# Kernel optimization log

Measured on AMD Instinct MI355X. Metric: run time of the kernel, lower is better.

Reference implementation:

```python
import jax, jax.numpy as jnp
import numpy as np

E_DIM = 64
N_EMBED = 8192

def setup_inputs() -> dict:
    key = jax.random.key(0)
    k1, k2 = jax.random.split(key)
    x = jax.random.normal(k1, (16, E_DIM, 32, 32), dtype=jnp.float32)   # [B, e_dim, H, W]
    embed = jax.random.normal(k2, (E_DIM, N_EMBED), dtype=jnp.float32)  # codebook [e_dim, n_embed]
    return {"x": x, "embed": embed}

def reference(x, embed):
    e_dim, n_embed = embed.shape
    # NCHW -> NHWC
    xp = jnp.transpose(x, (0, 2, 3, 1))              # [B, H, W, e_dim]
    flat = xp.reshape(-1, e_dim)                     # [N, e_dim]
    # squared-distance expansion: ||f||^2 - 2 f.E + ||e||^2  -> [N, n_embed]
    distance = (jnp.sum(flat * flat, axis=1, keepdims=True)
                - 2.0 * flat @ embed
                + jnp.sum(embed * embed, axis=0, keepdims=True))
    embed_idx = jnp.argmax(-distance, axis=1)        # [N] nearest code ids
    embed_idx = embed_idx.reshape(xp.shape[:-1])     # [B, H, W]
    # gather codes: embedding table is embed.T -> [n_embed, e_dim]
    quantize = jnp.take(embed.T, embed_idx, axis=0)  # [B, H, W, e_dim]
    return quantize
```

## Files before the change

### kernel.cpp

```cpp
#include <hip/hip_runtime.h>


typedef __attribute__((ext_vector_type(8))) __bf16 bf16x8;
typedef __attribute__((ext_vector_type(4))) float f32x4;
typedef unsigned int u32;
typedef unsigned long long u64;

union frag_cast { f32x4 f; bf16x8 b; };
__device__ __forceinline__ bf16x8 as_bf16x8(f32x4 v) { frag_cast u; u.f = v; return u.b; }

#define N_ROWS  16384
#define E_DIM   64
#define N_EMBED 8192
#define NCHUNK  16
#define COLS_PER_BLOCK (N_EMBED / NCHUNK)
#define N_ST (COLS_PER_BLOCK / 64)
#define ROWS_PER_BLOCK 512
#define N_ROWBLK (N_ROWS / ROWS_PER_BLOCK)
#define NT 8
#define MARGIN_THR 2e-3f

#define WS_AH   0u
#define WS_AL   (2u << 20)
#define WS_B    (4u << 20)
#define WS_ET   (6u << 20)
#define WS_BIAS (8u << 20)
#define WS_CNT  (WS_BIAS + (32u << 10))
#define WS_PB1  (WS_CNT + (4u << 10))
#define WS_PI1  (WS_PB1 + (1u << 20))
#define WS_PB2  (WS_PI1 + (1u << 20))
#define WS_FLAG (WS_PB2 + (1u << 20))
#define WS_FKEY (WS_FLAG + (64u << 10))
#define WS_DONE (WS_FKEY + (128u << 10))

__device__ __forceinline__ u32 f32_key(float s) {
    u32 u = __float_as_uint(s);
    return (u & 0x80000000u) ? ~u : (u | 0x80000000u);
}

__device__ __forceinline__ void async16(const void* g, void* l) {
    __builtin_amdgcn_global_load_lds(
        (const __attribute__((address_space(1))) void*)g,
        (__attribute__((address_space(3))) void*)l, 16, 0, 0);
}

__global__ __launch_bounds__(256) void prep(
        const float* __restrict__ x, const float* __restrict__ embed, char* ws) {
    __shared__ float tile[64][65];
    __bf16* Ah = (__bf16*)(ws + WS_AH);
    __bf16* Al = (__bf16*)(ws + WS_AL);
    float*  eT = (float*)(ws + WS_ET);
    float*  bias = (float*)(ws + WS_BIAS);
    const int t = threadIdx.x;
    const int blk = blockIdx.x;

    if (blk < 256) {
        const int b = blk >> 4, p0 = (blk & 15) * 64;
        {
            const int c = t >> 2, seg = (t & 3) * 16;
            const float* src = x + b * 65536 + c * 1024 + p0 + seg;
#pragma unroll
            for (int i = 0; i < 16; ++i) tile[c][seg + i] = src[i];
        }
        __syncthreads();
        const int p = t >> 2, cq = (t & 3) * 16;
        const long row = b * 1024 + p0 + p;
        bf16x8 vh0, vh1, vl0, vl1;
#pragma unroll
        for (int i = 0; i < 16; ++i) {
            float f = tile[cq + i][p];
            __bf16 h = (__bf16)f;
            __bf16 l = (__bf16)(f - (float)h);
            if (i < 8) { vh0[i] = h; vl0[i] = l; }
            else       { vh1[i - 8] = h; vl1[i - 8] = l; }
        }
        *(bf16x8*)(Ah + row * 64 + cq) = vh0;
        *(bf16x8*)(Ah + row * 64 + cq + 8) = vh1;
        *(bf16x8*)(Al + row * 64 + cq) = vl0;
        *(bf16x8*)(Al + row * 64 + cq + 8) = vl1;
    } else {
        if (blk == 256 && t == 0) *(int*)(ws + WS_CNT) = 0;
        const int g = blk - 256;
        const int jbase = g * 64;
        char* Bg = ws + WS_B + (size_t)g * 16384;
        {
            const int c = t >> 2, seg = (t & 3) * 16;
            const float* src = embed + c * N_EMBED + jbase + seg;
#pragma unroll
            for (int i = 0; i < 16; ++i) tile[c][seg + i] = src[i];
        }
        __syncthreads();
        if (t < 64) {
            float s = 0.f;
#pragma unroll
            for (int c = 0; c < 64; ++c) { float v = tile[c][t]; s = fmaf(v, v, s); }
            bias[jbase + t] = -0.5f * s;
        }
        const int jl = t >> 2, cq = (t & 3) * 16;
        bf16x8 vh0, vh1, vl0, vl1;
#pragma unroll
        for (int i = 0; i < 16; ++i) {
            float f = tile[cq + i][jl];
            eT[(long)(jbase + jl) * 64 + cq + i] = f;
            __bf16 h = (__bf16)f;
            __bf16 l = (__bf16)(f - (float)h);
            if (i < 8) { vh0[i] = h; vl0[i] = l; }
            else       { vh1[i - 8] = h; vl1[i - 8] = l; }
        }
        const int k0 = (cq >> 3), sw = jl & 7;
        __bf16* hi = (__bf16*)Bg + jl * 64;
        __bf16* lo = (__bf16*)(Bg + 8192) + jl * 64;
        *(bf16x8*)(hi + ((k0 ^ sw) * 8))       = vh0;
        *(bf16x8*)(hi + (((k0 + 1) ^ sw) * 8)) = vh1;
        *(bf16x8*)(lo + ((k0 ^ sw) * 8))       = vl0;
        *(bf16x8*)(lo + (((k0 + 1) ^ sw) * 8)) = vl1;
    }
}

__global__ __launch_bounds__(256, 2) void qdist(const char* __restrict__ ws_c, char* __restrict__ ws) {
    __shared__ __align__(16) char smem[2][16384];
    const __bf16* Ah = (const __bf16*)(ws_c + WS_AH);
    const __bf16* Al = (const __bf16*)(ws_c + WS_AL);
    const char* Bws = ws_c + WS_B;
    const float* biasg = (const float*)(ws_c + WS_BIAS);
    float* pb1 = (float*)(ws + WS_PB1);
    int*   pi1 = (int*)(ws + WS_PI1);
    float* pb2 = (float*)(ws + WS_PB2);

    const int t = threadIdx.x;
    const int wv = t >> 6, lane = t & 63, ln = lane & 15, q = lane >> 4;
    const int rb = blockIdx.x >> 4, chunk = blockIdx.x & 15;
    const int row0 = rb * ROWS_PER_BLOCK;
    const int col0 = chunk * COLS_PER_BLOCK;
    const int g0 = col0 >> 6;

    f32x4 pfh[NT][2], pfl[NT][2];
#pragma unroll
    for (int nt = 0; nt < NT; ++nt) {
        long row = row0 + wv * 128 + nt * 16 + ln;
        long base = row * 64 + q * 8;
        pfh[nt][0] = *(const f32x4*)(Ah + base);
        pfh[nt][1] = *(const f32x4*)(Ah + base + 32);
        pfl[nt][0] = *(const f32x4*)(Al + base);
        pfl[nt][1] = *(const f32x4*)(Al + base + 32);
    }
    asm volatile("" :
        "+v"(pfh[0][0]), "+v"(pfh[0][1]), "+v"(pfh[1][0]), "+v"(pfh[1][1]),
        "+v"(pfh[2][0]), "+v"(pfh[2][1]), "+v"(pfh[3][0]), "+v"(pfh[3][1]),
        "+v"(pfh[4][0]), "+v"(pfh[4][1]), "+v"(pfh[5][0]), "+v"(pfh[5][1]),
        "+v"(pfh[6][0]), "+v"(pfh[6][1]), "+v"(pfh[7][0]), "+v"(pfh[7][1]));
    asm volatile("" :
        "+v"(pfl[0][0]), "+v"(pfl[0][1]), "+v"(pfl[1][0]), "+v"(pfl[1][1]),
        "+v"(pfl[2][0]), "+v"(pfl[2][1]), "+v"(pfl[3][0]), "+v"(pfl[3][1]),
        "+v"(pfl[4][0]), "+v"(pfl[4][1]), "+v"(pfl[5][0]), "+v"(pfl[5][1]),
        "+v"(pfl[6][0]), "+v"(pfl[6][1]), "+v"(pfl[7][0]), "+v"(pfl[7][1]));

    float b1[NT], b2[NT]; int iq[NT];
#pragma unroll
    for (int k = 0; k < NT; ++k) { b1[k] = -3.4e38f; b2[k] = -3.4e38f; iq[k] = 0; }

    const int s7 = ln & 7;
    const int rdbase = ln * 128 + ((q ^ s7) << 4);

    auto issue = [&](int st) {
        const char* src = Bws + (size_t)(g0 + st) * 16384;
        char* dst = smem[st & 1];
#pragma unroll
        for (int s = 0; s < 4; ++s)
            async16(src + s * 4096 + wv * 1024 + lane * 16,
                    dst + s * 4096 + wv * 1024);
    };

    issue(0);
    for (int st = 0; st < N_ST; ++st) {
        __syncthreads();
        if (st + 1 < N_ST) issue(st + 1);
        const char* buf = smem[st & 1];
        __builtin_amdgcn_s_setprio(1);
#pragma unroll
        for (int ct = 0; ct < 4; ++ct) {
            const int boff = ct * 2048 + rdbase;
            bf16x8 ah0 = *(const bf16x8*)(buf + boff);
            bf16x8 ah1 = *(const bf16x8*)(buf + (boff ^ 64));
            bf16x8 al0 = *(const bf16x8*)(buf + 8192 + boff);
            bf16x8 al1 = *(const bf16x8*)(buf + 8192 + (boff ^ 64));
            const int cbase = col0 + st * 64 + ct * 16;
            f32x4 bv = *(const f32x4*)(biasg + cbase + q * 4);
            const int jq = cbase + q * 4;
#pragma unroll
            for (int nt = 0; nt < NT; ++nt) {
                f32x4 acc = __builtin_amdgcn_mfma_f32_16x16x32_bf16(al0, as_bf16x8(pfh[nt][0]), bv, 0, 0, 0);
                acc = __builtin_amdgcn_mfma_f32_16x16x32_bf16(al1, as_bf16x8(pfh[nt][1]), acc, 0, 0, 0);
                acc = __builtin_amdgcn_mfma_f32_16x16x32_bf16(ah0, as_bf16x8(pfl[nt][0]), acc, 0, 0, 0);
                acc = __builtin_amdgcn_mfma_f32_16x16x32_bf16(ah1, as_bf16x8(pfl[nt][1]), acc, 0, 0, 0);
                acc = __builtin_amdgcn_mfma_f32_16x16x32_bf16(ah0, as_bf16x8(pfh[nt][0]), acc, 0, 0, 0);
                acc = __builtin_amdgcn_mfma_f32_16x16x32_bf16(ah1, as_bf16x8(pfh[nt][1]), acc, 0, 0, 0);
                float mx = fmaxf(fmaxf(acc[0], acc[1]), fmaxf(acc[2], acc[3]));
                b2[nt] = fmaxf(b2[nt], fminf(b1[nt], mx));
                bool gt = mx > b1[nt];
                b1[nt] = fmaxf(b1[nt], mx);
                iq[nt] = gt ? jq : iq[nt];
            }
        }
        __builtin_amdgcn_s_setprio(0);
    }

#pragma unroll
    for (int m = 16; m < 64; m <<= 1) {
#pragma unroll
        for (int nt = 0; nt < NT; ++nt) {
            float o1 = __shfl_xor(b1[nt], m);
            int   oi = __shfl_xor(iq[nt], m);
            float o2 = __shfl_xor(b2[nt], m);
            b2[nt] = fmaxf(fmaxf(fminf(b1[nt], o1), o2), b2[nt]);
            bool take = (o1 > b1[nt]) || (o1 == b1[nt] && oi < iq[nt]);
            if (take) { b1[nt] = o1; iq[nt] = oi; }
        }
    }
    if (q == 0) {
#pragma unroll
        for (int nt = 0; nt < NT; ++nt) {
            int pixel = row0 + wv * 128 + nt * 16 + ln;
            int o = chunk * N_ROWS + pixel;
            pb1[o] = b1[nt];
            pi1[o] = iq[nt];
            pb2[o] = b2[nt];
        }
    }
}

__global__ __launch_bounds__(256) void reduce_rows(const float* __restrict__ x, char* ws,
                                                   float* __restrict__ out) {
    const float* pb1 = (const float*)(ws + WS_PB1);
    const int*   pi1 = (const int*)(ws + WS_PI1);
    const float* pb2 = (const float*)(ws + WS_PB2);
    const float* eT = (const float*)(ws + WS_ET);
    const float* bias = (const float*)(ws + WS_BIAS);
    int* flags = (int*)(ws + WS_FLAG);
    int* cnt = (int*)(ws + WS_CNT);
    u64* fkey = (u64*)(ws + WS_FKEY);
    int* done = (int*)(ws + WS_DONE);
    const int t = threadIdx.x;
    const int row = (blockIdx.x * 256 + t) >> 2;
    const int sub = t & 3;

    float m1 = -3.4e38f, m2 = -3.4e38f; int mi = 0;
#pragma unroll
    for (int k = 0; k < 4; ++k) {
        const int ch = sub * 4 + k;
        float o1 = pb1[ch * N_ROWS + row];
        int   oi = pi1[ch * N_ROWS + row];
        float o2 = pb2[ch * N_ROWS + row];
        m2 = fmaxf(fmaxf(fminf(m1, o1), o2), m2);
        if (o1 > m1 || (o1 == m1 && oi < mi)) { m1 = o1; mi = oi; }
    }
#pragma unroll
    for (int m = 1; m < 4; m <<= 1) {
        float o1 = __shfl_xor(m1, m);
        int   oi = __shfl_xor(mi, m);
        float o2 = __shfl_xor(m2, m);
        m2 = fmaxf(fmaxf(fminf(m1, o1), o2), m2);
        bool take = (o1 > m1) || (o1 == m1 && oi < mi);
        if (take) { m1 = o1; mi = oi; }
    }

    if (m1 - m2 < MARGIN_THR) {
        if (sub == 0) {
            fkey[row] = 0ull;
            done[row] = 0;
            flags[atomicAdd(cnt, 1)] = row;
        }
    } else {
        const float* xb = x + (row >> 10) * 65536 + (row & 1023);
        const int j = mi + sub;
        const f32x4* ecd = (const f32x4*)(eT + (size_t)j * 64);
        float s = bias[j];
#pragma unroll
        for (int v = 0; v < 16; ++v) {
            f32x4 ev = ecd[v];
            s = fmaf(xb[(v * 4 + 0) * 1024], ev[0], s);
            s = fmaf(xb[(v * 4 + 1) * 1024], ev[1], s);
            s = fmaf(xb[(v * 4 + 2) * 1024], ev[2], s);
            s = fmaf(xb[(v * 4 + 3) * 1024], ev[3], s);
        }
        float best = s; int bj = j;
#pragma unroll
        for (int m = 1; m < 4; m <<= 1) {
            float os = __shfl_xor(best, m);
            int   oj = __shfl_xor(bj, m);
            bool take = (os > best) || (os == best && oj < bj);
            if (take) { best = os; bj = oj; }
        }
        const f32x4* src = (const f32x4*)(eT + (size_t)bj * 64);
        f32x4* dst = (f32x4*)(out + (size_t)row * 64);
#pragma unroll
        for (int v = 0; v < 4; ++v) dst[v * 4 + sub] = src[v * 4 + sub];
    }
}

__global__ __launch_bounds__(256) void recheck(const float* __restrict__ x, char* ws,
                                               float* __restrict__ out) {
    __shared__ float fl[64];
    __shared__ u64 red[256];
    __shared__ int sLast, sIdx;
    const float* eT = (const float*)(ws + WS_ET);
    const float* bias = (const float*)(ws + WS_BIAS);
    const int* flags = (const int*)(ws + WS_FLAG);
    const int n = *(const int*)(ws + WS_CNT);
    u64* fkey = (u64*)(ws + WS_FKEY);
    int* done = (int*)(ws + WS_DONE);
    const int t = threadIdx.x;

    for (int e = blockIdx.x; e < n * 32; e += gridDim.x) {
        const int row = flags[e >> 5];
        const int seg = e & 31;
        __syncthreads();
        if (t < 64) fl[t] = x[(row >> 10) * 65536 + t * 1024 + (row & 1023)];
        __syncthreads();
        float xr[64];
#pragma unroll
        for (int c = 0; c < 64; ++c) xr[c] = fl[c];

        const int j = seg * 256 + t;
        const f32x4* ecd = (const f32x4*)(eT + (size_t)j * 64);
        f32x4 a0 = {0.f, 0.f, 0.f, 0.f}, a1 = a0, a2 = a0, a3 = a0;
#pragma unroll
        for (int v = 0; v < 4; ++v) {
            f32x4 e0 = ecd[v * 4 + 0], e1 = ecd[v * 4 + 1];
            f32x4 e2 = ecd[v * 4 + 2], e3 = ecd[v * 4 + 3];
#pragma unroll
            for (int k = 0; k < 4; ++k) {
                a0[k] = fmaf(xr[v * 16 + k],      e0[k], a0[k]);
                a1[k] = fmaf(xr[v * 16 + 4 + k],  e1[k], a1[k]);
                a2[k] = fmaf(xr[v * 16 + 8 + k],  e2[k], a2[k]);
                a3[k] = fmaf(xr[v * 16 + 12 + k], e3[k], a3[k]);
            }
        }
        f32x4 a01 = a0 + a1, a23 = a2 + a3;
        f32x4 as = a01 + a23;
        float s = bias[j] + ((as[0] + as[1]) + (as[2] + as[3]));

        red[t] = ((u64)f32_key(s) << 32) | (u32)(~(u32)j);
        __syncthreads();
        for (int off = 128; off; off >>= 1) {
            if (t < off) { u64 o = red[t + off]; if (o > red[t]) red[t] = o; }
            __syncthreads();
        }
        if (t == 0) {
            atomicMax(&fkey[row], red[0]);
            __threadfence();
            sLast = (atomicAdd(&done[row], 1) == 31) ? 1 : 0;
        }
        __syncthreads();
        if (sLast) {
            if (t == 0) {
                u64 k = atomicMax(&fkey[row], 0ull);
                sIdx = (int)(~(u32)(k & 0xffffffffull));
            }
            __syncthreads();
            if (t < 64) out[(size_t)row * 64 + t] = eT[(size_t)sIdx * 64 + t];
        }
        __syncthreads();
    }
}

extern "C" void kernel_launch(void* const* d_in, const int* in_sizes, int n_in,
                              void* d_out, int out_size, void* d_ws, size_t ws_size,
                              hipStream_t stream) {
    const float* x     = (const float*)d_in[0];
    const float* embed = (const float*)d_in[1];
    float* out = (float*)d_out;
    char* ws = (char*)d_ws;

    prep<<<384, 256, 0, stream>>>(x, embed, ws);
    qdist<<<N_ROWBLK * NCHUNK, 256, 0, stream>>>(ws, ws);
    reduce_rows<<<256, 256, 0, stream>>>(x, ws, out);
    recheck<<<2048, 256, 0, stream>>>(x, ws, out);
}
```

Baseline: 129.1 us.

## Fuse distance, row-reduce and recheck kernels into one persistent kernel with grid barriers

```diff
diff --git a/kernel.cpp b/kernel.cpp
--- a/kernel.cpp
+++ b/kernel.cpp
@@ -19,6 +19,7 @@
 #define N_ROWBLK (N_ROWS / ROWS_PER_BLOCK)
 #define NT 8
 #define MARGIN_THR 2e-3f
+#define FUSED_GRID 512
 
 #define WS_AH   0u
 #define WS_AL   (2u << 20)
@@ -44,6 +45,23 @@
         (__attribute__((address_space(3))) void*)l, 16, 0, 0);
 }
 
+__device__ __forceinline__ void grid_sync(int* cnt, int* gen) {
+    __threadfence();
+    __syncthreads();
+    if (threadIdx.x == 0) {
+        int g = atomicAdd(gen, 0);
+        if (atomicAdd(cnt, 1) == FUSED_GRID - 1) {
+            atomicExch(cnt, 0);
+            __threadfence();
+            atomicAdd(gen, 1);
+        } else {
+            while (atomicAdd(gen, 0) == g) __builtin_amdgcn_s_sleep(2);
+        }
+    }
+    __syncthreads();
+    __threadfence();
+}
+
 __global__ __launch_bounds__(256) void prep(
         const float* __restrict__ x, const float* __restrict__ embed, char* ws) {
     __shared__ float tile[64][65];
@@ -79,7 +97,12 @@
         *(bf16x8*)(Al + row * 64 + cq) = vl0;
         *(bf16x8*)(Al + row * 64 + cq + 8) = vl1;
     } else {
-        if (blk == 256 && t == 0) *(int*)(ws + WS_CNT) = 0;
+        if (blk == 256 && t == 0) {
+            int* cnt = (int*)(ws + WS_CNT);
+            cnt[0] = 0;
+            cnt[2] = 0;
+            cnt[3] = 0;
+        }
         const int g = blk - 256;
         const int jbase = g * 64;
         char* Bg = ws + WS_B + (size_t)g * 16384;
@@ -117,250 +140,251 @@
     }
 }
 
-__global__ __launch_bounds__(256, 2) void qdist(const char* __restrict__ ws_c, char* __restrict__ ws) {
+__global__ __launch_bounds__(256, 2) void fused(const char* __restrict__ ws_c, char* ws,
+                                                const float* __restrict__ x,
+                                                float* __restrict__ out) {
     __shared__ __align__(16) char smem[2][16384];
+    __shared__ float fl[64];
+    __shared__ u64 red[256];
+    __shared__ int sLast, sIdx, sN;
     const __bf16* Ah = (const __bf16*)(ws_c + WS_AH);
     const __bf16* Al = (const __bf16*)(ws_c + WS_AL);
     const char* Bws = ws_c + WS_B;
     const float* biasg = (const float*)(ws_c + WS_BIAS);
+    const float* eT = (const float*)(ws_c + WS_ET);
     float* pb1 = (float*)(ws + WS_PB1);
     int*   pi1 = (int*)(ws + WS_PI1);
     float* pb2 = (float*)(ws + WS_PB2);
-
-    const int t = threadIdx.x;
-    const int wv = t >> 6, lane = t & 63, ln = lane & 15, q = lane >> 4;
-    const int rb = blockIdx.x >> 4, chunk = blockIdx.x & 15;
-    const int row0 = rb * ROWS_PER_BLOCK;
-    const int col0 = chunk * COLS_PER_BLOCK;
-    const int g0 = col0 >> 6;
-
-    f32x4 pfh[NT][2], pfl[NT][2];
-#pragma unroll
-    for (int nt = 0; nt < NT; ++nt) {
-        long row = row0 + wv * 128 + nt * 16 + ln;
-        long base = row * 64 + q * 8;
-        pfh[nt][0] = *(const f32x4*)(Ah + base);
-        pfh[nt][1] = *(const f32x4*)(Ah + base + 32);
-        pfl[nt][0] = *(const f32x4*)(Al + base);
-        pfl[nt][1] = *(const f32x4*)(Al + base + 32);
-    }
-    asm volatile("" :
-        "+v"(pfh[0][0]), "+v"(pfh[0][1]), "+v"(pfh[1][0]), "+v"(pfh[1][1]),
-        "+v"(pfh[2][0]), "+v"(pfh[2][1]), "+v"(pfh[3][0]), "+v"(pfh[3][1]),
-        "+v"(pfh[4][0]), "+v"(pfh[4][1]), "+v"(pfh[5][0]), "+v"(pfh[5][1]),
-        "+v"(pfh[6][0]), "+v"(pfh[6][1]), "+v"(pfh[7][0]), "+v"(pfh[7][1]));
-    asm volatile("" :
-        "+v"(pfl[0][0]), "+v"(pfl[0][1]), "+v"(pfl[1][0]), "+v"(pfl[1][1]),
-        "+v"(pfl[2][0]), "+v"(pfl[2][1]), "+v"(pfl[3][0]), "+v"(pfl[3][1]),
-        "+v"(pfl[4][0]), "+v"(pfl[4][1]), "+v"(pfl[5][0]), "+v"(pfl[5][1]),
-        "+v"(pfl[6][0]), "+v"(pfl[6][1]), "+v"(pfl[7][0]), "+v"(pfl[7][1]));
-
-    float b1[NT], b2[NT]; int iq[NT];
-#pragma unroll
-    for (int k = 0; k < NT; ++k) { b1[k] = -3.4e38f; b2[k] = -3.4e38f; iq[k] = 0; }
-
-    const int s7 = ln & 7;
-    const int rdbase = ln * 128 + ((q ^ s7) << 4);
-
-    auto issue = [&](int st) {
-        const char* src = Bws + (size_t)(g0 + st) * 16384;
-        char* dst = smem[st & 1];
-#pragma unroll
-        for (int s = 0; s < 4; ++s)
-            async16(src + s * 4096 + wv * 1024 + lane * 16,
-                    dst + s * 4096 + wv * 1024);
-    };
-
-    issue(0);
-    for (int st = 0; st < N_ST; ++st) {
-        __syncthreads();
-        if (st + 1 < N_ST) issue(st + 1);
-        const char* buf = smem[st & 1];
-        __builtin_amdgcn_s_setprio(1);
-#pragma unroll
-        for (int ct = 0; ct < 4; ++ct) {
-            const int boff = ct * 2048 + rdbase;
-            bf16x8 ah0 = *(const bf16x8*)(buf + boff);
-            bf16x8 ah1 = *(const bf16x8*)(buf + (boff ^ 64));
-            bf16x8 al0 = *(const bf16x8*)(buf + 8192 + boff);
-            bf16x8 al1 = *(const bf16x8*)(buf + 8192 + (boff ^ 64));
-            const int cbase = col0 + st * 64 + ct * 16;
-            f32x4 bv = *(const f32x4*)(biasg + cbase + q * 4);
-            const int jq = cbase + q * 4;
-#pragma unroll
-            for (int nt = 0; nt < NT; ++nt) {
-                f32x4 acc = __builtin_amdgcn_mfma_f32_16x16x32_bf16(al0, as_bf16x8(pfh[nt][0]), bv, 0, 0, 0);
-                acc = __builtin_amdgcn_mfma_f32_16x16x32_bf16(al1, as_bf16x8(pfh[nt][1]), acc, 0, 0, 0);
-                acc = __builtin_amdgcn_mfma_f32_16x16x32_bf16(ah0, as_bf16x8(pfl[nt][0]), acc, 0, 0, 0);
-                acc = __builtin_amdgcn_mfma_f32_16x16x32_bf16(ah1, as_bf16x8(pfl[nt][1]), acc, 0, 0, 0);
-                acc = __builtin_amdgcn_mfma_f32_16x16x32_bf16(ah0, as_bf16x8(pfh[nt][0]), acc, 0, 0, 0);
-                acc = __builtin_amdgcn_mfma_f32_16x16x32_bf16(ah1, as_bf16x8(pfh[nt][1]), acc, 0, 0, 0);
-                float mx = fmaxf(fmaxf(acc[0], acc[1]), fmaxf(acc[2], acc[3]));
-                b2[nt] = fmaxf(b2[nt], fminf(b1[nt], mx));
-                bool gt = mx > b1[nt];
-                b1[nt] = fmaxf(b1[nt], mx);
-                iq[nt] = gt ? jq : iq[nt];
-            }
-        }
-        __builtin_amdgcn_s_setprio(0);
-    }
-
-#pragma unroll
-    for (int m = 16; m < 64; m <<= 1) {
-#pragma unroll
-        for (int nt = 0; nt < NT; ++nt) {
-            float o1 = __shfl_xor(b1[nt], m);
-            int   oi = __shfl_xor(iq[nt], m);
-            float o2 = __shfl_xor(b2[nt], m);
-            b2[nt] = fmaxf(fmaxf(fminf(b1[nt], o1), o2), b2[nt]);
-            bool take = (o1 > b1[nt]) || (o1 == b1[nt] && oi < iq[nt]);
-            if (take) { b1[nt] = o1; iq[nt] = oi; }
-        }
-    }
-    if (q == 0) {
-#pragma unroll
-        for (int nt = 0; nt < NT; ++nt) {
-            int pixel = row0 + wv * 128 + nt * 16 + ln;
-            int o = chunk * N_ROWS + pixel;
-            pb1[o] = b1[nt];
-            pi1[o] = iq[nt];
-            pb2[o] = b2[nt];
-        }
-    }
-}
-
-__global__ __launch_bounds__(256) void reduce_rows(const float* __restrict__ x, char* ws,
-                                                   float* __restrict__ out) {
-    const float* pb1 = (const float*)(ws + WS_PB1);
-    const int*   pi1 = (const int*)(ws + WS_PI1);
-    const float* pb2 = (const float*)(ws + WS_PB2);
-    const float* eT = (const float*)(ws + WS_ET);
-    const float* bias = (const float*)(ws + WS_BIAS);
     int* flags = (int*)(ws + WS_FLAG);
     int* cnt = (int*)(ws + WS_CNT);
     u64* fkey = (u64*)(ws + WS_FKEY);
     int* done = (int*)(ws + WS_DONE);
+
     const int t = threadIdx.x;
-    const int row = (blockIdx.x * 256 + t) >> 2;
-    const int sub = t & 3;
-
-    float m1 = -3.4e38f, m2 = -3.4e38f; int mi = 0;
-#pragma unroll
-    for (int k = 0; k < 4; ++k) {
-        const int ch = sub * 4 + k;
-        float o1 = pb1[ch * N_ROWS + row];
-        int   oi = pi1[ch * N_ROWS + row];
-        float o2 = pb2[ch * N_ROWS + row];
-        m2 = fmaxf(fmaxf(fminf(m1, o1), o2), m2);
-        if (o1 > m1 || (o1 == m1 && oi < mi)) { m1 = o1; mi = oi; }
+
+    {
+        const int wv = t >> 6, lane = t & 63, ln = lane & 15, q = lane >> 4;
+        const int rb = blockIdx.x >> 4, chunk = blockIdx.x & 15;
+        const int row0 = rb * ROWS_PER_BLOCK;
+        const int col0 = chunk * COLS_PER_BLOCK;
+        const int g0 = col0 >> 6;
+
+        f32x4 pfh[NT][2], pfl[NT][2];
+#pragma unroll
+        for (int nt = 0; nt < NT; ++nt) {
+            long row = row0 + wv * 128 + nt * 16 + ln;
+            long base = row * 64 + q * 8;
+            pfh[nt][0] = *(const f32x4*)(Ah + base);
+            pfh[nt][1] = *(const f32x4*)(Ah + base + 32);
+            pfl[nt][0] = *(const f32x4*)(Al + base);
+            pfl[nt][1] = *(const f32x4*)(Al + base + 32);
+        }
+        asm volatile("" :
+            "+v"(pfh[0][0]), "+v"(pfh[0][1]), "+v"(pfh[1][0]), "+v"(pfh[1][1]),
+            "+v"(pfh[2][0]), "+v"(pfh[2][1]), "+v"(pfh[3][0]), "+v"(pfh[3][1]),
+            "+v"(pfh[4][0]), "+v"(pfh[4][1]), "+v"(pfh[5][0]), "+v"(pfh[5][1]),
+            "+v"(pfh[6][0]), "+v"(pfh[6][1]), "+v"(pfh[7][0]), "+v"(pfh[7][1]));
+        asm volatile("" :
+            "+v"(pfl[0][0]), "+v"(pfl[0][1]), "+v"(pfl[1][0]), "+v"(pfl[1][1]),
+            "+v"(pfl[2][0]), "+v"(pfl[2][1]), "+v"(pfl[3][0]), "+v"(pfl[3][1]),
+            "+v"(pfl[4][0]), "+v"(pfl[4][1]), "+v"(pfl[5][0]), "+v"(pfl[5][1]),
+            "+v"(pfl[6][0]), "+v"(pfl[6][1]), "+v"(pfl[7][0]), "+v"(pfl[7][1]));
+
+        float b1[NT], b2[NT]; int iq[NT];
+#pragma unroll
+        for (int k = 0; k < NT; ++k) { b1[k] = -3.4e38f; b2[k] = -3.4e38f; iq[k] = 0; }
+
+        const int s7 = ln & 7;
+        const int rdbase = ln * 128 + ((q ^ s7) << 4);
+
+        auto issue = [&](int st) {
+            const char* src = Bws + (size_t)(g0 + st) * 16384;
+            char* dst = smem[st & 1];
+#pragma unroll
+            for (int s = 0; s < 4; ++s)
+                async16(src + s * 4096 + wv * 1024 + lane * 16,
+                        dst + s * 4096 + wv * 1024);
+        };
+
+        issue(0);
+        for (int st = 0; st < N_ST; ++st) {
+            __syncthreads();
+            if (st + 1 < N_ST) issue(st + 1);
+            const char* buf = smem[st & 1];
+            __builtin_amdgcn_s_setprio(1);
+#pragma unroll
+            for (int ct = 0; ct < 4; ++ct) {
+                const int boff = ct * 2048 + rdbase;
+                bf16x8 ah0 = *(const bf16x8*)(buf + boff);
+                bf16x8 ah1 = *(const bf16x8*)(buf + (boff ^ 64));
+                bf16x8 al0 = *(const bf16x8*)(buf + 8192 + boff);
+                bf16x8 al1 = *(const bf16x8*)(buf + 8192 + (boff ^ 64));
+                const int cbase = col0 + st * 64 + ct * 16;
+                f32x4 bv = *(const f32x4*)(biasg + cbase + q * 4);
+                const int jq = cbase + q * 4;
+#pragma unroll
+                for (int nt = 0; nt < NT; ++nt) {
+                    f32x4 acc = __builtin_amdgcn_mfma_f32_16x16x32_bf16(al0, as_bf16x8(pfh[nt][0]), bv, 0, 0, 0);
+                    acc = __builtin_amdgcn_mfma_f32_16x16x32_bf16(al1, as_bf16x8(pfh[nt][1]), acc, 0, 0, 0);
+                    acc = __builtin_amdgcn_mfma_f32_16x16x32_bf16(ah0, as_bf16x8(pfl[nt][0]), acc, 0, 0, 0);
+                    acc = __builtin_amdgcn_mfma_f32_16x16x32_bf16(ah1, as_bf16x8(pfl[nt][1]), acc, 0, 0, 0);
+                    acc = __builtin_amdgcn_mfma_f32_16x16x32_bf16(ah0, as_bf16x8(pfh[nt][0]), acc, 0, 0, 0);
+                    acc = __builtin_amdgcn_mfma_f32_16x16x32_bf16(ah1, as_bf16x8(pfh[nt][1]), acc, 0, 0, 0);
+                    float mx = fmaxf(fmaxf(acc[0], acc[1]), fmaxf(acc[2], acc[3]));
+                    b2[nt] = fmaxf(b2[nt], fminf(b1[nt], mx));
+                    bool gt = mx > b1[nt];
+                    b1[nt] = fmaxf(b1[nt], mx);
+                    iq[nt] = gt ? jq : iq[nt];
+                }
+            }
+            __builtin_amdgcn_s_setprio(0);
+        }
+
+#pragma unroll
+        for (int m = 16; m < 64; m <<= 1) {
+#pragma unroll
+            for (int nt = 0; nt < NT; ++nt) {
+                float o1 = __shfl_xor(b1[nt], m);
+                int   oi = __shfl_xor(iq[nt], m);
+                float o2 = __shfl_xor(b2[nt], m);
+                b2[nt] = fmaxf(fmaxf(fminf(b1[nt], o1), o2), b2[nt]);
+                bool take = (o1 > b1[nt]) || (o1 == b1[nt] && oi < iq[nt]);
+                if (take) { b1[nt] = o1; iq[nt] = oi; }
+            }
+        }
+        if (q == 0) {
+#pragma unroll
+            for (int nt = 0; nt < NT; ++nt) {
+                int pixel = row0 + wv * 128 + nt * 16 + ln;
+                int o = chunk * N_ROWS + pixel;
+                pb1[o] = b1[nt];
+                pi1[o] = iq[nt];
+                pb2[o] = b2[nt];
+            }
+        }
     }
-#pragma unroll
-    for (int m = 1; m < 4; m <<= 1) {
-        float o1 = __shfl_xor(m1, m);
-        int   oi = __shfl_xor(mi, m);
-        float o2 = __shfl_xor(m2, m);
-        m2 = fmaxf(fmaxf(fminf(m1, o1), o2), m2);
-        bool take = (o1 > m1) || (o1 == m1 && oi < mi);
-        if (take) { m1 = o1; mi = oi; }
+
+    grid_sync(cnt + 2, cnt + 3);
+
+    {
+        const float* bias = biasg;
+        const int sub = t & 7;
+        const int row = blockIdx.x * 32 + (t >> 3);
+        float m1 = -3.4e38f, m2 = -3.4e38f; int mi = 0;
+#pragma unroll
+        for (int k = 0; k < 2; ++k) {
+            const int ch = sub * 2 + k;
+            float o1 = pb1[ch * N_ROWS + row];
+            int   oi = pi1[ch * N_ROWS + row];
+            float o2 = pb2[ch * N_ROWS + row];
+            m2 = fmaxf(fmaxf(fminf(m1, o1), o2), m2);
+            if (o1 > m1 || (o1 == m1 && oi < mi)) { m1 = o1; mi = oi; }
+        }
+#pragma unroll
+        for (int m = 1; m < 8; m <<= 1) {
+            float o1 = __shfl_xor(m1, m);
+            int   oi = __shfl_xor(mi, m);
+            float o2 = __shfl_xor(m2, m);
+            m2 = fmaxf(fmaxf(fminf(m1, o1), o2), m2);
+            bool take = (o1 > m1) || (o1 == m1 && oi < mi);
+            if (take) { m1 = o1; mi = oi; }
+        }
+
+        if (m1 - m2 < MARGIN_THR) {
+            if (sub == 0) {
+                fkey[row] = 0ull;
+                done[row] = 0;
+                flags[atomicAdd(cnt, 1)] = row;
+            }
+        } else {
+            const float* xb = x + (row >> 10) * 65536 + (row & 1023);
+            const int j = mi + (sub & 3);
+            const int h = sub >> 2;
+            const f32x4* ecd = (const f32x4*)(eT + (size_t)j * 64) + h * 8;
+            float s = h ? 0.f : bias[j];
+#pragma unroll
+            for (int v = 0; v < 8; ++v) {
+                f32x4 ev = ecd[v];
+                const int c0 = h * 32 + v * 4;
+                s = fmaf(xb[(c0 + 0) * 1024], ev[0], s);
+                s = fmaf(xb[(c0 + 1) * 1024], ev[1], s);
+                s = fmaf(xb[(c0 + 2) * 1024], ev[2], s);
+                s = fmaf(xb[(c0 + 3) * 1024], ev[3], s);
+            }
+            s += __shfl_xor(s, 4);
+            float best = s; int bj = j;
+#pragma unroll
+            for (int m = 1; m < 4; m <<= 1) {
+                float os = __shfl_xor(best, m);
+                int   oj = __shfl_xor(bj, m);
+                bool take = (os > best) || (os == best && oj < bj);
+                if (take) { best = os; bj = oj; }
+            }
+            const f32x4* src = (const f32x4*)(eT + (size_t)bj * 64);
+            f32x4* dst = (f32x4*)(out + (size_t)row * 64);
+            dst[sub] = src[sub];
+            dst[sub + 8] = src[sub + 8];
+        }
     }
 
-    if (m1 - m2 < MARGIN_THR) {
-        if (sub == 0) {
-            fkey[row] = 0ull;
-            done[row] = 0;
-            flags[atomicAdd(cnt, 1)] = row;
-        }
-    } else {
-        const float* xb = x + (row >> 10) * 65536 + (row & 1023);
-        const int j = mi + sub;
-        const f32x4* ecd = (const f32x4*)(eT + (size_t)j * 64);
-        float s = bias[j];
-#pragma unroll
-        for (int v = 0; v < 16; ++v) {
-            f32x4 ev = ecd[v];
-            s = fmaf(xb[(v * 4 + 0) * 1024], ev[0], s);
-            s = fmaf(xb[(v * 4 + 1) * 1024], ev[1], s);
-            s = fmaf(xb[(v * 4 + 2) * 1024], ev[2], s);
-            s = fmaf(xb[(v * 4 + 3) * 1024], ev[3], s);
-        }
-        float best = s; int bj = j;
-#pragma unroll
-        for (int m = 1; m < 4; m <<= 1) {
-            float os = __shfl_xor(best, m);
-            int   oj = __shfl_xor(bj, m);
-            bool take = (os > best) || (os == best && oj < bj);
-            if (take) { best = os; bj = oj; }
-        }
-        const f32x4* src = (const f32x4*)(eT + (size_t)bj * 64);
-        f32x4* dst = (f32x4*)(out + (size_t)row * 64);
-#pragma unroll
-        for (int v = 0; v < 4; ++v) dst[v * 4 + sub] = src[v * 4 + sub];
-    }
-}
-
-__global__ __launch_bounds__(256) void recheck(const float* __restrict__ x, char* ws,
-                                               float* __restrict__ out) {
-    __shared__ float fl[64];
-    __shared__ u64 red[256];
-    __shared__ int sLast, sIdx;
-    const float* eT = (const float*)(ws + WS_ET);
-    const float* bias = (const float*)(ws + WS_BIAS);
-    const int* flags = (const int*)(ws + WS_FLAG);
-    const int n = *(const int*)(ws + WS_CNT);
-    u64* fkey = (u64*)(ws + WS_FKEY);
-    int* done = (int*)(ws + WS_DONE);
-    const int t = threadIdx.x;
-
-    for (int e = blockIdx.x; e < n * 32; e += gridDim.x) {
-        const int row = flags[e >> 5];
-        const int seg = e & 31;
+    grid_sync(cnt + 2, cnt + 3);
+
+    {
+        const float* bias = biasg;
+        if (t == 0) sN = atomicAdd(cnt, 0);
         __syncthreads();
-        if (t < 64) fl[t] = x[(row >> 10) * 65536 + t * 1024 + (row & 1023)];
-        __syncthreads();
-        float xr[64];
-#pragma unroll
-        for (int c = 0; c < 64; ++c) xr[c] = fl[c];
-
-        const int j = seg * 256 + t;
-        const f32x4* ecd = (const f32x4*)(eT + (size_t)j * 64);
-        f32x4 a0 = {0.f, 0.f, 0.f, 0.f}, a1 = a0, a2 = a0, a3 = a0;
-#pragma unroll
-        for (int v = 0; v < 4; ++v) {
-            f32x4 e0 = ecd[v * 4 + 0], e1 = ecd[v * 4 + 1];
-            f32x4 e2 = ecd[v * 4 + 2], e3 = ecd[v * 4 + 3];
-#pragma unroll
-            for (int k = 0; k < 4; ++k) {
-                a0[k] = fmaf(xr[v * 16 + k],      e0[k], a0[k]);
-                a1[k] = fmaf(xr[v * 16 + 4 + k],  e1[k], a1[k]);
-                a2[k] = fmaf(xr[v * 16 + 8 + k],  e2[k], a2[k]);
-                a3[k] = fmaf(xr[v * 16 + 12 + k], e3[k], a3[k]);
-            }
-        }
-        f32x4 a01 = a0 + a1, a23 = a2 + a3;
-        f32x4 as = a01 + a23;
-        float s = bias[j] + ((as[0] + as[1]) + (as[2] + as[3]));
-
-        red[t] = ((u64)f32_key(s) << 32) | (u32)(~(u32)j);
-        __syncthreads();
-        for (int off = 128; off; off >>= 1) {
-            if (t < off) { u64 o = red[t + off]; if (o > red[t]) red[t] = o; }
-            __syncthreads();
-        }
-        if (t == 0) {
-            atomicMax(&fkey[row], red[0]);
-            __threadfence();
-            sLast = (atomicAdd(&done[row], 1) == 31) ? 1 : 0;
-        }
-        __syncthreads();
-        if (sLast) {
+        const int n = sN;
+        for (int e = blockIdx.x; e < n * 32; e += FUSED_GRID) {
+            const int row = flags[e >> 5];
+            const int seg = e & 31;
+            __syncthreads();
+            if (t < 64) fl[t] = x[(row >> 10) * 65536 + t * 1024 + (row & 1023)];
+            __syncthreads();
+            float xr[64];
+#pragma unroll
+            for (int c = 0; c < 64; ++c) xr[c] = fl[c];
+
+            const int j = seg * 256 + t;
+            const f32x4* ecd = (const f32x4*)(eT + (size_t)j * 64);
+            f32x4 a0 = {0.f, 0.f, 0.f, 0.f}, a1 = a0, a2 = a0, a3 = a0;
+#pragma unroll
+            for (int v = 0; v < 4; ++v) {
+                f32x4 e0 = ecd[v * 4 + 0], e1 = ecd[v * 4 + 1];
+                f32x4 e2 = ecd[v * 4 + 2], e3 = ecd[v * 4 + 3];
+#pragma unroll
+                for (int k = 0; k < 4; ++k) {
+                    a0[k] = fmaf(xr[v * 16 + k],      e0[k], a0[k]);
+                    a1[k] = fmaf(xr[v * 16 + 4 + k],  e1[k], a1[k]);
+                    a2[k] = fmaf(xr[v * 16 + 8 + k],  e2[k], a2[k]);
+                    a3[k] = fmaf(xr[v * 16 + 12 + k], e3[k], a3[k]);
+                }
+            }
+            f32x4 a01 = a0 + a1, a23 = a2 + a3;
+            f32x4 as = a01 + a23;
+            float s = bias[j] + ((as[0] + as[1]) + (as[2] + as[3]));
+
+            red[t] = ((u64)f32_key(s) << 32) | (u32)(~(u32)j);
+            __syncthreads();
+            for (int off = 128; off; off >>= 1) {
+                if (t < off) { u64 o = red[t + off]; if (o > red[t]) red[t] = o; }
+                __syncthreads();
+            }
             if (t == 0) {
-                u64 k = atomicMax(&fkey[row], 0ull);
-                sIdx = (int)(~(u32)(k & 0xffffffffull));
-            }
-            __syncthreads();
-            if (t < 64) out[(size_t)row * 64 + t] = eT[(size_t)sIdx * 64 + t];
-        }
-        __syncthreads();
+                atomicMax(&fkey[row], red[0]);
+                __threadfence();
+                sLast = (atomicAdd(&done[row], 1) == 31) ? 1 : 0;
+            }
+            __syncthreads();
+            if (sLast) {
+                if (t == 0) {
+                    u64 k = atomicMax(&fkey[row], 0ull);
+                    sIdx = (int)(~(u32)(k & 0xffffffffull));
+                }
+                __syncthreads();
+                if (t < 64) out[(size_t)row * 64 + t] = eT[(size_t)sIdx * 64 + t];
+            }
+            __syncthreads();
+        }
     }
 }
 
@@ -373,7 +397,5 @@
     char* ws = (char*)d_ws;
 
     prep<<<384, 256, 0, stream>>>(x, embed, ws);
-    qdist<<<N_ROWBLK * NCHUNK, 256, 0, stream>>>(ws, ws);
-    reduce_rows<<<256, 256, 0, stream>>>(x, ws, out);
-    recheck<<<2048, 256, 0, stream>>>(x, ws, out);
-}
+    fused<<<FUSED_GRID, 256, 0, stream>>>(ws, ws, x, out);
+}
```

New measurement: 335.0 us. +159.5%, slower.

## Fold ambiguous-row recheck into reduce_rows with per-wave chunk pruning

Applied to the files above, without the earlier changes.

```diff
diff --git a/kernel.cpp b/kernel.cpp
--- a/kernel.cpp
+++ b/kernel.cpp
@@ -29,9 +29,6 @@
 #define WS_PB1  (WS_CNT + (4u << 10))
 #define WS_PI1  (WS_PB1 + (1u << 20))
 #define WS_PB2  (WS_PI1 + (1u << 20))
-#define WS_FLAG (WS_PB2 + (1u << 20))
-#define WS_FKEY (WS_FLAG + (64u << 10))
-#define WS_DONE (WS_FKEY + (128u << 10))
 
 __device__ __forceinline__ u32 f32_key(float s) {
     u32 u = __float_as_uint(s);
@@ -79,7 +76,6 @@
         *(bf16x8*)(Al + row * 64 + cq) = vl0;
         *(bf16x8*)(Al + row * 64 + cq + 8) = vl1;
     } else {
-        if (blk == 256 && t == 0) *(int*)(ws + WS_CNT) = 0;
         const int g = blk - 256;
         const int jbase = g * 64;
         char* Bg = ws + WS_B + (size_t)g * 16384;
@@ -236,11 +232,8 @@
     const float* pb2 = (const float*)(ws + WS_PB2);
     const float* eT = (const float*)(ws + WS_ET);
     const float* bias = (const float*)(ws + WS_BIAS);
-    int* flags = (int*)(ws + WS_FLAG);
-    int* cnt = (int*)(ws + WS_CNT);
-    u64* fkey = (u64*)(ws + WS_FKEY);
-    int* done = (int*)(ws + WS_DONE);
     const int t = threadIdx.x;
+    const int lane = t & 63, wv = t >> 6;
     const int row = (blockIdx.x * 256 + t) >> 2;
     const int sub = t & 3;
 
@@ -264,13 +257,8 @@
         if (take) { m1 = o1; mi = oi; }
     }
 
-    if (m1 - m2 < MARGIN_THR) {
-        if (sub == 0) {
-            fkey[row] = 0ull;
-            done[row] = 0;
-            flags[atomicAdd(cnt, 1)] = row;
-        }
-    } else {
+    const bool flagged = (m1 - m2 < MARGIN_THR);
+    if (!flagged) {
         const float* xb = x + (row >> 10) * 65536 + (row & 1023);
         const int j = mi + sub;
         const f32x4* ecd = (const f32x4*)(eT + (size_t)j * 64);
@@ -296,71 +284,56 @@
 #pragma unroll
         for (int v = 0; v < 4; ++v) dst[v * 4 + sub] = src[v * 4 + sub];
     }
-}
-
-__global__ __launch_bounds__(256) void recheck(const float* __restrict__ x, char* ws,
-                                               float* __restrict__ out) {
-    __shared__ float fl[64];
-    __shared__ u64 red[256];
-    __shared__ int sLast, sIdx;
-    const float* eT = (const float*)(ws + WS_ET);
-    const float* bias = (const float*)(ws + WS_BIAS);
-    const int* flags = (const int*)(ws + WS_FLAG);
-    const int n = *(const int*)(ws + WS_CNT);
-    u64* fkey = (u64*)(ws + WS_FKEY);
-    int* done = (int*)(ws + WS_DONE);
-    const int t = threadIdx.x;
-
-    for (int e = blockIdx.x; e < n * 32; e += gridDim.x) {
-        const int row = flags[e >> 5];
-        const int seg = e & 31;
-        __syncthreads();
-        if (t < 64) fl[t] = x[(row >> 10) * 65536 + t * 1024 + (row & 1023)];
-        __syncthreads();
+
+    u64 bal = __ballot(flagged);
+    const int wrow0 = blockIdx.x * 64 + wv * 16;
+    while (bal) {
+        const int b = __ffsll(bal) - 1;
+        const int rw = b >> 2;
+        bal &= ~(0xFull << (rw * 4));
+        const int r = wrow0 + rw;
+        const float rb1 = __shfl(m1, rw * 4);
+        const float cutoff = rb1 - 2.0f * MARGIN_THR;
+
+        float xv = x[(r >> 10) * 65536 + lane * 1024 + (r & 1023)];
         float xr[64];
 #pragma unroll
-        for (int c = 0; c < 64; ++c) xr[c] = fl[c];
-
-        const int j = seg * 256 + t;
-        const f32x4* ecd = (const f32x4*)(eT + (size_t)j * 64);
-        f32x4 a0 = {0.f, 0.f, 0.f, 0.f}, a1 = a0, a2 = a0, a3 = a0;
-#pragma unroll
-        for (int v = 0; v < 4; ++v) {
-            f32x4 e0 = ecd[v * 4 + 0], e1 = ecd[v * 4 + 1];
-            f32x4 e2 = ecd[v * 4 + 2], e3 = ecd[v * 4 + 3];
-#pragma unroll
-            for (int k = 0; k < 4; ++k) {
-                a0[k] = fmaf(xr[v * 16 + k],      e0[k], a0[k]);
-                a1[k] = fmaf(xr[v * 16 + 4 + k],  e1[k], a1[k]);
-                a2[k] = fmaf(xr[v * 16 + 8 + k],  e2[k], a2[k]);
-                a3[k] = fmaf(xr[v * 16 + 12 + k], e3[k], a3[k]);
+        for (int c = 0; c < 64; ++c) xr[c] = __shfl(xv, c);
+
+        u64 bestk = 0ull;
+        for (int ch = 0; ch < NCHUNK; ++ch) {
+            if (pb1[ch * N_ROWS + r] < cutoff) continue;
+#pragma unroll
+            for (int k = 0; k < 8; ++k) {
+                const int j = ch * 512 + lane * 8 + k;
+                const f32x4* ecd = (const f32x4*)(eT + (size_t)j * 64);
+                f32x4 a0 = {0.f, 0.f, 0.f, 0.f}, a1 = a0, a2 = a0, a3 = a0;
+#pragma unroll
+                for (int v = 0; v < 4; ++v) {
+                    f32x4 e0 = ecd[v * 4 + 0], e1 = ecd[v * 4 + 1];
+                    f32x4 e2 = ecd[v * 4 + 2], e3 = ecd[v * 4 + 3];
+#pragma unroll
+                    for (int kk = 0; kk < 4; ++kk) {
+                        a0[kk] = fmaf(xr[v * 16 + kk],      e0[kk], a0[kk]);
+                        a1[kk] = fmaf(xr[v * 16 + 4 + kk],  e1[kk], a1[kk]);
+                        a2[kk] = fmaf(xr[v * 16 + 8 + kk],  e2[kk], a2[kk]);
+                        a3[kk] = fmaf(xr[v * 16 + 12 + kk], e3[kk], a3[kk]);
+                    }
+                }
+                f32x4 a01 = a0 + a1, a23 = a2 + a3;
+                f32x4 as = a01 + a23;
+                float s = bias[j] + ((as[0] + as[1]) + (as[2] + as[3]));
+                u64 key = ((u64)f32_key(s) << 32) | (u32)(~(u32)j);
+                bestk = (key > bestk) ? key : bestk;
             }
         }
-        f32x4 a01 = a0 + a1, a23 = a2 + a3;
-        f32x4 as = a01 + a23;
-        float s = bias[j] + ((as[0] + as[1]) + (as[2] + as[3]));
-
-        red[t] = ((u64)f32_key(s) << 32) | (u32)(~(u32)j);
-        __syncthreads();
-        for (int off = 128; off; off >>= 1) {
-            if (t < off) { u64 o = red[t + off]; if (o > red[t]) red[t] = o; }
-            __syncthreads();
-        }
-        if (t == 0) {
-            atomicMax(&fkey[row], red[0]);
-            __threadfence();
-            sLast = (atomicAdd(&done[row], 1) == 31) ? 1 : 0;
-        }
-        __syncthreads();
-        if (sLast) {
-            if (t == 0) {
-                u64 k = atomicMax(&fkey[row], 0ull);
-                sIdx = (int)(~(u32)(k & 0xffffffffull));
-            }
-            __syncthreads();
-            if (t < 64) out[(size_t)row * 64 + t] = eT[(size_t)sIdx * 64 + t];
-        }
-        __syncthreads();
+#pragma unroll
+        for (int m = 1; m < 64; m <<= 1) {
+            u64 o = __shfl_xor(bestk, m);
+            bestk = (o > bestk) ? o : bestk;
+        }
+        const int idx = (int)(~(u32)(bestk & 0xffffffffull));
+        out[(size_t)r * 64 + lane] = eT[(size_t)idx * 64 + lane];
     }
 }
 
@@ -375,5 +348,4 @@
     prep<<<384, 256, 0, stream>>>(x, embed, ws);
     qdist<<<N_ROWBLK * NCHUNK, 256, 0, stream>>>(ws, ws);
     reduce_rows<<<256, 256, 0, stream>>>(x, ws, out);
-    recheck<<<2048, 256, 0, stream>>>(x, ws, out);
-}
+}
```

Result: no change. 130.2 us (+0.9%).
